# Optimization experiments

Hardware: AMD Instinct MI355X
Metric: run time of the kernel (lower is better)

## Reference

```python
import jax, jax.numpy as jnp
import numpy as np

B, H, W, C = 2, 64, 64, 256
NH, K = 8, 7  # num_heads, neighborhood kernel size


def setup_inputs() -> dict:
    key = jax.random.key(0)
    ks = jax.random.split(key, 8)
    xav = lambda k, shape: jax.random.normal(k, shape, jnp.float32) * np.sqrt(2.0 / (shape[0] + shape[1])).astype(np.float32)
    return {
        "x": jax.random.normal(ks[0], (B, H, W, C), jnp.float32),
        "norm1_g": jnp.ones((C,), jnp.float32),
        "norm1_b": jnp.zeros((C,), jnp.float32),
        "qkv_w": xav(ks[1], (3 * C, C)),
        "qkv_b": jnp.zeros((3 * C,), jnp.float32),
        "rpb": jax.random.normal(ks[2], (NH, 2 * K - 1, 2 * K - 1), jnp.float32) * 0.02,
        "proj_w": xav(ks[3], (C, C)),
        "proj_b": jnp.zeros((C,), jnp.float32),
        "norm2_g": jnp.ones((C,), jnp.float32),
        "norm2_b": jnp.zeros((C,), jnp.float32),
        "fc1_w": xav(ks[4], (4 * C, C)),
        "fc1_b": jnp.zeros((4 * C,), jnp.float32),
        "fc2_w": xav(ks[5], (C, 4 * C)),
        "fc2_b": jnp.zeros((C,), jnp.float32),
    }


def _layernorm(x, g, b, eps=1e-5):
    m = x.mean(-1, keepdims=True)
    v = jnp.mean((x - m) ** 2, axis=-1, keepdims=True)
    return (x - m) * jax.lax.rsqrt(v + eps) * g + b


def _nat2d(x, qkv_w, qkv_b, rpb, proj_w, proj_b):
    """Neighborhood attention 2D (NATTEN semantics: edge-clamped k x k windows,
    relative positional bias indexed by key_pos - query_pos + k - 1)."""
    b, h, w, c = x.shape
    nh = rpb.shape[0]
    k = (rpb.shape[1] + 1) // 2
    dh = c // nh
    qkv = (x @ qkv_w.T + qkv_b).reshape(b, h, w, 3, nh, dh)
    q = qkv[..., 0, :, :] * (dh ** -0.5)  # [b,h,w,nh,dh]
    kk = qkv[..., 1, :, :]
    vv = qkv[..., 2, :, :]
    # edge-clamped window starts per query row/col
    starts_h = jnp.clip(jnp.arange(h) - k // 2, 0, h - k)
    starts_w = jnp.clip(jnp.arange(w) - k // 2, 0, w - k)
    idx_h = starts_h[:, None] + jnp.arange(k)  # [h,k] key row indices
    idx_w = starts_w[:, None] + jnp.arange(k)  # [w,k] key col indices
    # gather neighborhoods -> [b,h,w,k,k,nh,dh]
    knb = kk[:, idx_h][:, :, :, idx_w].transpose(0, 1, 3, 2, 4, 5, 6)
    vnb = vv[:, idx_h][:, :, :, idx_w].transpose(0, 1, 3, 2, 4, 5, 6)
    attn = jnp.einsum('bijhd,bijklhd->bijhkl', q, knb)  # [b,h,w,nh,k,k]
    # relative positional bias: index = key - query + (k-1) in [0, 2k-2]
    rb_h = idx_h - jnp.arange(h)[:, None] + (k - 1)  # [h,k]
    rb_w = idx_w - jnp.arange(w)[:, None] + (k - 1)  # [w,k]
    bias = rpb[:, rb_h][:, :, :, rb_w]  # [nh,h,k,w,k]
    bias = bias.transpose(1, 3, 0, 2, 4)  # [h,w,nh,k,k]
    attn = jax.nn.softmax((attn + bias).reshape(b, h, w, nh, k * k), axis=-1)
    out = jnp.einsum('bijhn,bijnhd->bijhd', attn, vnb.reshape(b, h, w, k * k, nh, dh))
    return out.reshape(b, h, w, c) @ proj_w.T + proj_b


def reference(x, norm1_g, norm1_b, qkv_w, qkv_b, rpb, proj_w, proj_b,
              norm2_g, norm2_b, fc1_w, fc1_b, fc2_w, fc2_b):
    # norm -> neighborhood attention -> residual
    x = x + _nat2d(_layernorm(x, norm1_g, norm1_b), qkv_w, qkv_b, rpb, proj_w, proj_b)
    # norm -> MLP (gelu) -> residual
    hdn = _layernorm(x, norm2_g, norm2_b)
    hdn = jax.nn.gelu(hdn @ fc1_w.T + fc1_b, approximate=False)
    return x + (hdn @ fc2_w.T + fc2_b)
```

## Files before the change

kernel.cpp:

```cpp
#include <hip/hip_runtime.h>

typedef __attribute__((ext_vector_type(8))) short bf16x8;
typedef __attribute__((ext_vector_type(4))) float f32x4;
typedef unsigned short u16;

__device__ __forceinline__ float bf2f(u16 u) {
    return __builtin_bit_cast(float, ((unsigned int)u) << 16);
}
__device__ __forceinline__ u16 f2bf(float f) {
    unsigned int x = __builtin_bit_cast(unsigned int, f);
    x += 0x7FFFu + ((x >> 16) & 1u);
    return (u16)(x >> 16);
}

typedef const __attribute__((address_space(1))) void* gas_t;
typedef __attribute__((address_space(3))) void* las_t;
__device__ __forceinline__ void load_lds16(const u16* g, u16* l) {
    __builtin_amdgcn_global_load_lds((gas_t)g, (las_t)l, 16, 0, 0);
}

__global__ __launch_bounds__(256) void prep_kernel(
    const float* __restrict__ s0, const float* __restrict__ s1,
    const float* __restrict__ s2, const float* __restrict__ s3,
    u16* __restrict__ dst,
    const float* __restrict__ x, const float* __restrict__ g,
    const float* __restrict__ b, u16* __restrict__ y)
{
    if (blockIdx.x < 768) {
        const int i4 = (blockIdx.x * 256 + threadIdx.x) * 4;
        const float* src;
        int off;
        if      (i4 < 196608) { src = s0; off = i4; }
        else if (i4 < 262144) { src = s1; off = i4 - 196608; }
        else if (i4 < 524288) { src = s2; off = i4 - 262144; }
        else                  { src = s3; off = i4 - 524288; }
        float4 v = *(const float4*)(src + off);
        ushort4 o;
        o.x = f2bf(v.x); o.y = f2bf(v.y); o.z = f2bf(v.z); o.w = f2bf(v.w);
        *(ushort4*)(dst + i4) = o;
        return;
    }
    const int tok  = (blockIdx.x - 768) * 4 + (threadIdx.x >> 6);
    const int lane = threadIdx.x & 63;
    float4 v = *(const float4*)(x + (size_t)tok * 256 + lane * 4);
    float s  = v.x + v.y + v.z + v.w;
    float sq = v.x*v.x + v.y*v.y + v.z*v.z + v.w*v.w;
    #pragma unroll
    for (int off = 32; off; off >>= 1) {
        s  += __shfl_xor(s, off);
        sq += __shfl_xor(sq, off);
    }
    float mean = s * (1.0f / 256.0f);
    float var  = sq * (1.0f / 256.0f) - mean * mean;
    float rs   = rsqrtf(var + 1e-5f);
    float4 gv = *(const float4*)(g + lane * 4);
    float4 bv = *(const float4*)(b + lane * 4);
    ushort4 o;
    o.x = f2bf((v.x - mean) * rs * gv.x + bv.x);
    o.y = f2bf((v.y - mean) * rs * gv.y + bv.y);
    o.z = f2bf((v.z - mean) * rs * gv.z + bv.z);
    o.w = f2bf((v.w - mean) * rs * gv.w + bv.w);
    *(ushort4*)(y + (size_t)tok * 256 + lane * 4) = o;
}

template<int BM, int BN, int N, int K, int EPI>
__global__ __launch_bounds__(256) void gemm(
    const u16* __restrict__ A, const u16* __restrict__ W,
    const float* __restrict__ bias, const float* __restrict__ res,
    void* __restrict__ outv,
    const float* __restrict__ g2, const float* __restrict__ b2,
    u16* __restrict__ out2)
{
    constexpr int WMT = BM / 32;
    constexpr int WNT = BN / 32;
    constexpr int AR  = BM / 32;
    constexpr int BR  = BN / 32;

    __shared__ u16 As[BM * 64];
    __shared__ u16 Bs[BN * 64];
    __shared__ float red[2][2][16][2];
    const int tid  = threadIdx.x;
    const int lane = tid & 63;
    const int wave = tid >> 6;
    const int m0   = blockIdx.x * BM;
    const int n0   = blockIdx.y * BN;
    const int wm0  = (wave >> 1) * (BM / 2);
    const int wn0  = (wave & 1) * (BN / 2);

    f32x4 acc[WMT][WNT];
    #pragma unroll
    for (int mt = 0; mt < WMT; ++mt)
        #pragma unroll
        for (int nt = 0; nt < WNT; ++nt)
            acc[mt][nt] = (f32x4){0.f, 0.f, 0.f, 0.f};

    int soffA[AR];
    #pragma unroll
    for (int r = 0; r < AR; ++r) {
        const int s   = r * 256 + tid;
        const int row = s >> 3;
        const int c   = (s & 7) ^ (row & 7);
        soffA[r] = row * K + c * 8;
    }
    int soffB[BR];
    #pragma unroll
    for (int r = 0; r < BR; ++r) {
        const int s   = r * 256 + tid;
        const int row = s >> 3;
        const int c   = (s & 7) ^ (row & 7);
        soffB[r] = row * K + c * 8;
    }
    const int fr = lane & 15;
    const int fc = lane >> 4;

    for (int k0 = 0; k0 < K; k0 += 64) {
        __syncthreads();
        #pragma unroll
        for (int r = 0; r < AR; ++r)
            load_lds16(A + (size_t)m0 * K + k0 + soffA[r], As + (r * 256 + tid) * 8);
        #pragma unroll
        for (int r = 0; r < BR; ++r)
            load_lds16(W + (size_t)n0 * K + k0 + soffB[r], Bs + (r * 256 + tid) * 8);
        __syncthreads();
        #pragma unroll
        for (int ks = 0; ks < 2; ++ks) {
            bf16x8 af[WMT], bw[WNT];
            #pragma unroll
            for (int mt = 0; mt < WMT; ++mt) {
                const int rr   = wm0 + mt * 16 + fr;
                const int phys = (ks * 4 + fc) ^ (rr & 7);
                af[mt] = *(const bf16x8*)(As + rr * 64 + phys * 8);
            }
            #pragma unroll
            for (int nt = 0; nt < WNT; ++nt) {
                const int rr   = wn0 + nt * 16 + fr;
                const int phys = (ks * 4 + fc) ^ (rr & 7);
                bw[nt] = *(const bf16x8*)(Bs + rr * 64 + phys * 8);
            }
            #pragma unroll
            for (int mt = 0; mt < WMT; ++mt)
                #pragma unroll
                for (int nt = 0; nt < WNT; ++nt)
                    acc[mt][nt] = __builtin_amdgcn_mfma_f32_16x16x32_bf16(af[mt], bw[nt], acc[mt][nt], 0, 0, 0);
        }
    }

    const int col = lane & 15;
    const int rb  = (lane >> 4) * 4;

    if (EPI == 4) {
        float vv[WNT][4];
        float s[4]  = {0.f, 0.f, 0.f, 0.f};
        float sq[4] = {0.f, 0.f, 0.f, 0.f};
        #pragma unroll
        for (int nt = 0; nt < WNT; ++nt) {
            const int n  = n0 + wn0 + nt * 16 + col;
            const float bv = bias[n];
            #pragma unroll
            for (int r = 0; r < 4; ++r) {
                const int m = m0 + wm0 + rb + r;
                float v = acc[0][nt][r] + bv + res[(size_t)m * N + n];
                ((float*)outv)[(size_t)m * N + n] = v;
                vv[nt][r] = v;
                s[r]  += v;
                sq[r] += v * v;
            }
        }
        #pragma unroll
        for (int off = 1; off < 16; off <<= 1) {
            #pragma unroll
            for (int r = 0; r < 4; ++r) {
                s[r]  += __shfl_xor(s[r], off);
                sq[r] += __shfl_xor(sq[r], off);
            }
        }
        if ((lane & 15) == 0) {
            #pragma unroll
            for (int r = 0; r < 4; ++r) {
                red[wave >> 1][wave & 1][rb + r][0] = s[r];
                red[wave >> 1][wave & 1][rb + r][1] = sq[r];
            }
        }
        __syncthreads();
        float mean[4], rs[4];
        #pragma unroll
        for (int r = 0; r < 4; ++r) {
            float ts  = red[wave >> 1][0][rb + r][0] + red[wave >> 1][1][rb + r][0];
            float tsq = red[wave >> 1][0][rb + r][1] + red[wave >> 1][1][rb + r][1];
            mean[r] = ts * (1.0f / 256.0f);
            float var = tsq * (1.0f / 256.0f) - mean[r] * mean[r];
            rs[r] = rsqrtf(var + 1e-5f);
        }
        #pragma unroll
        for (int nt = 0; nt < WNT; ++nt) {
            const int n  = n0 + wn0 + nt * 16 + col;
            const float gv = g2[n];
            const float bv2 = b2[n];
            #pragma unroll
            for (int r = 0; r < 4; ++r) {
                const int m = m0 + wm0 + rb + r;
                out2[(size_t)m * 256 + n] = f2bf((vv[nt][r] - mean[r]) * rs[r] * gv + bv2);
            }
        }
        return;
    }

    #pragma unroll
    for (int nt = 0; nt < WNT; ++nt) {
        const int n  = n0 + wn0 + nt * 16 + col;
        const float bv = bias[n];
        #pragma unroll
        for (int mt = 0; mt < WMT; ++mt) {
            #pragma unroll
            for (int r = 0; r < 4; ++r) {
                const int m = m0 + wm0 + mt * 16 + rb + r;
                float v = acc[mt][nt][r] + bv;
                if (EPI == 1) {
                    if (n < 256) v *= 0.1767766952966369f;
                    ((u16*)outv)[(size_t)m * N + n] = f2bf(v);
                }
                if (EPI == 2) {
                    v += res[(size_t)m * N + n];
                    ((float*)outv)[(size_t)m * N + n] = v;
                }
                if (EPI == 3) {
                    v = 0.5f * v * (1.0f + erff(v * 0.7071067811865475f));
                    ((u16*)outv)[(size_t)m * N + n] = f2bf(v);
                }
            }
        }
    }
}

__global__ __launch_bounds__(64) void attn_mfma_kernel(
    const u16* __restrict__ qkv, const float* __restrict__ rpb,
    u16* __restrict__ out)
{
    __shared__ float rpbs[192];

    const int l = threadIdx.x;
    const int B = blockIdx.x;
    const int L = (B & 7) * 512 + (B >> 3);
    const int tile = L >> 3;
    const int h    = L & 7;
    const int bb   = tile >> 8;
    const int rem  = tile & 255;
    const int ti0  = (rem >> 4) << 2;
    const int tj0  = (rem & 15) << 2;
    const int oh   = min(max(ti0 - 3, 0), 54);
    const int ow   = min(max(tj0 - 3, 0), 54);
    const int tokbase = bb * 4096;

    #pragma unroll
    for (int r = 0; r < 3; ++r) {
        const int idx = r * 64 + l;
        rpbs[idx] = (idx < 169) ? rpb[h * 169 + idx] : -1e30f;
    }

    const int q = l & 15;
    const int g = l >> 4;

    const int tokq = tokbase + (ti0 + (q >> 2)) * 64 + (tj0 + (q & 3));
    const bf16x8 qf = *(const bf16x8*)(qkv + (size_t)tokq * 768 + h * 32 + g * 8);
    bf16x8 kf[7];
    #pragma unroll
    for (int t = 0; t < 7; ++t) {
        const int key = 16 * t + q;
        const int kkc = min(key, 99);
        const int tr  = (kkc * 205) >> 11, tc = kkc - tr * 10;
        const int tokg = tokbase + (oh + tr) * 64 + (ow + tc);
        kf[t] = *(const bf16x8*)(qkv + (size_t)tokg * 768 + 256 + h * 32 + g * 8);
    }

    const int i  = ti0 + (q >> 2), j = tj0 + (q & 3);
    const int sh = min(max(i - 3, 0), 57), sw = min(max(j - 3, 0), 57);
    const int khb = sh - oh, kwb = sw - ow;
    const int bh0 = oh - i + 6, bw0 = ow - j + 6;
    int bidx[7][4];
    int vtok[7][4];
    #pragma unroll
    for (int t = 0; t < 7; ++t)
        #pragma unroll
        for (int r = 0; r < 4; ++r) {
            const int kk  = 16 * t + 4 * g + r;
            const int kkc = min(kk, 99);
            const int hr  = (kkc * 205) >> 11;
            const int hc  = kkc - hr * 10;
            vtok[t][r] = tokbase + (oh + hr) * 64 + (ow + hc);
            const bool valid = (kk < 100)
                && ((unsigned)(hr - khb) < 7u) && ((unsigned)(hc - kwb) < 7u);
            bidx[t][r] = valid ? (bh0 + hr) * 13 + (bw0 + hc) : 169;
        }

    __syncthreads();

    f32x4 S[7];
    #pragma unroll
    for (int t = 0; t < 7; ++t)
        S[t] = __builtin_amdgcn_mfma_f32_16x16x32_bf16(kf[t], qf, (f32x4){0.f,0.f,0.f,0.f}, 0, 0, 0);

    float p[7][4];
    float mx = -1e30f;
    #pragma unroll
    for (int t = 0; t < 7; ++t)
        #pragma unroll
        for (int r = 0; r < 4; ++r) {
            const float v = S[t][r] + rpbs[bidx[t][r]];
            p[t][r] = v;
            mx = fmaxf(mx, v);
        }
    mx = fmaxf(mx, __shfl_xor(mx, 16));
    mx = fmaxf(mx, __shfl_xor(mx, 32));
    float sum = 0.f;
    #pragma unroll
    for (int t = 0; t < 7; ++t)
        #pragma unroll
        for (int r = 0; r < 4; ++r) {
            const float e = __expf(p[t][r] - mx);
            p[t][r] = e;
            sum += e;
        }
    sum += __shfl_xor(sum, 16);
    sum += __shfl_xor(sum, 32);
    const float inv = 1.f / sum;

    f32x4 O0 = {0.f,0.f,0.f,0.f}, O1 = {0.f,0.f,0.f,0.f};
    const u16* vbase = qkv + 512 + h * 32 + q;
    #pragma unroll
    for (int kt = 0; kt < 4; ++kt) {
        const int t0   = 2 * kt;
        const bool has1 = (2 * kt + 1) < 7;
        const int t1   = has1 ? 2 * kt + 1 : 2 * kt;
        bf16x8 ph, pl, vA, vB;
        #pragma unroll
        for (int jj = 0; jj < 4; ++jj) {
            const float a = p[t0][jj] * inv;
            const u16 ha = f2bf(a);
            ph[jj] = (short)ha;
            pl[jj] = (short)f2bf(a - bf2f(ha));
            const float b = has1 ? p[t1][jj] * inv : 0.f;
            const u16 hb = f2bf(b);
            ph[4 + jj] = (short)hb;
            pl[4 + jj] = (short)f2bf(b - bf2f(hb));
            vA[jj]     = (short)vbase[(size_t)vtok[t0][jj] * 768];
            vB[jj]     = (short)vbase[(size_t)vtok[t0][jj] * 768 + 16];
            vA[4 + jj] = (short)vbase[(size_t)vtok[t1][jj] * 768];
            vB[4 + jj] = (short)vbase[(size_t)vtok[t1][jj] * 768 + 16];
        }
        O0 = __builtin_amdgcn_mfma_f32_16x16x32_bf16(ph, vA, O0, 0, 0, 0);
        O0 = __builtin_amdgcn_mfma_f32_16x16x32_bf16(pl, vA, O0, 0, 0, 0);
        O1 = __builtin_amdgcn_mfma_f32_16x16x32_bf16(ph, vB, O1, 0, 0, 0);
        O1 = __builtin_amdgcn_mfma_f32_16x16x32_bf16(pl, vB, O1, 0, 0, 0);
    }

    #pragma unroll
    for (int r = 0; r < 4; ++r) {
        const int qq = g * 4 + r;
        const size_t base = (size_t)(tokbase + (ti0 + (qq >> 2)) * 64 + (tj0 + (qq & 3))) * 256
                          + h * 32 + q;
        out[base]      = f2bf(O0[r]);
        out[base + 16] = f2bf(O1[r]);
    }
}

extern "C" void kernel_launch(void* const* d_in, const int* in_sizes, int n_in,
                              void* d_out, int out_size, void* d_ws, size_t ws_size,
                              hipStream_t stream)
{
    const float* x      = (const float*)d_in[0];
    const float* n1g    = (const float*)d_in[1];
    const float* n1b    = (const float*)d_in[2];
    const float* qkv_w  = (const float*)d_in[3];
    const float* qkv_b  = (const float*)d_in[4];
    const float* rpb    = (const float*)d_in[5];
    const float* proj_w = (const float*)d_in[6];
    const float* proj_b = (const float*)d_in[7];
    const float* n2g    = (const float*)d_in[8];
    const float* n2b    = (const float*)d_in[9];
    const float* fc1_w  = (const float*)d_in[10];
    const float* fc1_b  = (const float*)d_in[11];
    const float* fc2_w  = (const float*)d_in[12];
    const float* fc2_b  = (const float*)d_in[13];
    float* out = (float*)d_out;

    char* wsb = (char*)d_ws;
    u16*   wbf   = (u16*)wsb;
    u16*   qkvW  = wbf;
    u16*   projW = wbf + 196608;
    u16*   fc1W  = wbf + 262144;
    u16*   fc2W  = wbf + 524288;
    u16*   ln1   = (u16*)(wsb + 1572864);
    u16*   attn  = ln1;
    u16*   qkvB  = (u16*)(wsb + 5767168);
    u16*   ln2   = qkvB;
    u16*   hbuf  = (u16*)(wsb + 9961472);
    float* x1    = (float*)(wsb + 26738688);

    dim3 blk(256);
    prep_kernel<<<2816, blk, 0, stream>>>(qkv_w, proj_w, fc1_w, fc2_w, wbf,
                                          x, n1g, n1b, ln1);
    gemm<128, 64, 768, 256, 1><<<dim3(64, 12), blk, 0, stream>>>(ln1, qkvW, qkv_b, nullptr, qkvB, nullptr, nullptr, nullptr);
    attn_mfma_kernel<<<4096, dim3(64), 0, stream>>>(qkvB, rpb, attn);
    gemm<32, 256, 256, 256, 4><<<dim3(256, 1), blk, 0, stream>>>(attn, projW, proj_b, x, x1, n2g, n2b, ln2);
    gemm<128, 64, 1024, 256, 3><<<dim3(64, 16), blk, 0, stream>>>(ln2, fc1W, fc1_b, nullptr, hbuf, nullptr, nullptr, nullptr);
    gemm<128, 64, 256, 1024, 2><<<dim3(64, 4), blk, 0, stream>>>(hbuf, fc2W, fc2_b, x1, out, nullptr, nullptr, nullptr);
}
```

Baseline: 151.4 us.

## Fuse neighborhood attention with output projection, residual and LayerNorm2

Merges the attention kernel with the projection GEMM epilogue. Each 512-thread block handles one 4x4 query tile, with 8 waves covering all heads. The attention output goes into swizzled LDS and is multiplied by projW, read directly from global memory. The block then adds bias and residual and computes LayerNorm2 in place. This removes a kernel launch and the global round trip of the attention output. In exchange there are fewer, larger blocks (512), and the projection weights are re-read from global memory by every block without LDS staging.

```diff
diff --git a/kernel.cpp b/kernel.cpp
--- a/kernel.cpp
+++ b/kernel.cpp
@@ -67,9 +67,7 @@
 __global__ __launch_bounds__(256) void gemm(
     const u16* __restrict__ A, const u16* __restrict__ W,
     const float* __restrict__ bias, const float* __restrict__ res,
-    void* __restrict__ outv,
-    const float* __restrict__ g2, const float* __restrict__ b2,
-    u16* __restrict__ out2)
+    void* __restrict__ outv)
 {
     constexpr int WMT = BM / 32;
     constexpr int WNT = BN / 32;
@@ -78,7 +76,6 @@
 
     __shared__ u16 As[BM * 64];
     __shared__ u16 Bs[BN * 64];
-    __shared__ float red[2][2][16][2];
     const int tid  = threadIdx.x;
     const int lane = tid & 63;
     const int wave = tid >> 6;
@@ -147,64 +144,6 @@
 
     const int col = lane & 15;
     const int rb  = (lane >> 4) * 4;
-
-    if (EPI == 4) {
-        float vv[WNT][4];
-        float s[4]  = {0.f, 0.f, 0.f, 0.f};
-        float sq[4] = {0.f, 0.f, 0.f, 0.f};
-        #pragma unroll
-        for (int nt = 0; nt < WNT; ++nt) {
-            const int n  = n0 + wn0 + nt * 16 + col;
-            const float bv = bias[n];
-            #pragma unroll
-            for (int r = 0; r < 4; ++r) {
-                const int m = m0 + wm0 + rb + r;
-                float v = acc[0][nt][r] + bv + res[(size_t)m * N + n];
-                ((float*)outv)[(size_t)m * N + n] = v;
-                vv[nt][r] = v;
-                s[r]  += v;
-                sq[r] += v * v;
-            }
-        }
-        #pragma unroll
-        for (int off = 1; off < 16; off <<= 1) {
-            #pragma unroll
-            for (int r = 0; r < 4; ++r) {
-                s[r]  += __shfl_xor(s[r], off);
-                sq[r] += __shfl_xor(sq[r], off);
-            }
-        }
-        if ((lane & 15) == 0) {
-            #pragma unroll
-            for (int r = 0; r < 4; ++r) {
-                red[wave >> 1][wave & 1][rb + r][0] = s[r];
-                red[wave >> 1][wave & 1][rb + r][1] = sq[r];
-            }
-        }
-        __syncthreads();
-        float mean[4], rs[4];
-        #pragma unroll
-        for (int r = 0; r < 4; ++r) {
-            float ts  = red[wave >> 1][0][rb + r][0] + red[wave >> 1][1][rb + r][0];
-            float tsq = red[wave >> 1][0][rb + r][1] + red[wave >> 1][1][rb + r][1];
-            mean[r] = ts * (1.0f / 256.0f);
-            float var = tsq * (1.0f / 256.0f) - mean[r] * mean[r];
-            rs[r] = rsqrtf(var + 1e-5f);
-        }
-        #pragma unroll
-        for (int nt = 0; nt < WNT; ++nt) {
-            const int n  = n0 + wn0 + nt * 16 + col;
-            const float gv = g2[n];
-            const float bv2 = b2[n];
-            #pragma unroll
-            for (int r = 0; r < 4; ++r) {
-                const int m = m0 + wm0 + rb + r;
-                out2[(size_t)m * 256 + n] = f2bf((vv[nt][r] - mean[r]) * rs[r] * gv + bv2);
-            }
-        }
-        return;
-    }
-
     #pragma unroll
     for (int nt = 0; nt < WNT; ++nt) {
         const int n  = n0 + wn0 + nt * 16 + col;
@@ -232,17 +171,22 @@
     }
 }
 
-__global__ __launch_bounds__(64) void attn_mfma_kernel(
+__global__ __launch_bounds__(512) void attn_proj_kernel(
     const u16* __restrict__ qkv, const float* __restrict__ rpb,
-    u16* __restrict__ out)
+    const u16* __restrict__ projW, const float* __restrict__ proj_b,
+    const float* __restrict__ xres, const float* __restrict__ g2,
+    const float* __restrict__ b2, float* __restrict__ x1,
+    u16* __restrict__ ln2)
 {
-    __shared__ float rpbs[192];
-
-    const int l = threadIdx.x;
-    const int B = blockIdx.x;
-    const int L = (B & 7) * 512 + (B >> 3);
-    const int tile = L >> 3;
-    const int h    = L & 7;
+    __shared__ u16   ao[16 * 256];
+    __shared__ float rpbs[8 * 177];
+    __shared__ float red[8][16][2];
+
+    const int tid = threadIdx.x;
+    const int l   = tid & 63;
+    const int w   = tid >> 6;
+    const int B   = blockIdx.x;
+    const int tile = (B & 7) * 64 + (B >> 3);
     const int bb   = tile >> 8;
     const int rem  = tile & 255;
     const int ti0  = (rem >> 4) << 2;
@@ -253,15 +197,19 @@
 
     #pragma unroll
     for (int r = 0; r < 3; ++r) {
-        const int idx = r * 64 + l;
-        rpbs[idx] = (idx < 169) ? rpb[h * 169 + idx] : -1e30f;
+        const int idx = r * 512 + tid;
+        if (idx < 1416) {
+            const int hh = idx / 177;
+            const int ii = idx - hh * 177;
+            rpbs[idx] = (ii < 169) ? rpb[hh * 169 + ii] : -1e30f;
+        }
     }
 
     const int q = l & 15;
     const int g = l >> 4;
 
     const int tokq = tokbase + (ti0 + (q >> 2)) * 64 + (tj0 + (q & 3));
-    const bf16x8 qf = *(const bf16x8*)(qkv + (size_t)tokq * 768 + h * 32 + g * 8);
+    const bf16x8 qf = *(const bf16x8*)(qkv + (size_t)tokq * 768 + w * 32 + g * 8);
     bf16x8 kf[7];
     #pragma unroll
     for (int t = 0; t < 7; ++t) {
@@ -269,7 +217,7 @@
         const int kkc = min(key, 99);
         const int tr  = (kkc * 205) >> 11, tc = kkc - tr * 10;
         const int tokg = tokbase + (oh + tr) * 64 + (ow + tc);
-        kf[t] = *(const bf16x8*)(qkv + (size_t)tokg * 768 + 256 + h * 32 + g * 8);
+        kf[t] = *(const bf16x8*)(qkv + (size_t)tokg * 768 + 256 + w * 32 + g * 8);
     }
 
     const int i  = ti0 + (q >> 2), j = tj0 + (q & 3);
@@ -299,13 +247,14 @@
     for (int t = 0; t < 7; ++t)
         S[t] = __builtin_amdgcn_mfma_f32_16x16x32_bf16(kf[t], qf, (f32x4){0.f,0.f,0.f,0.f}, 0, 0, 0);
 
+    const float* rpbh = rpbs + w * 177;
     float p[7][4];
     float mx = -1e30f;
     #pragma unroll
     for (int t = 0; t < 7; ++t)
         #pragma unroll
         for (int r = 0; r < 4; ++r) {
-            const float v = S[t][r] + rpbs[bidx[t][r]];
+            const float v = S[t][r] + rpbh[bidx[t][r]];
             p[t][r] = v;
             mx = fmaxf(mx, v);
         }
@@ -325,7 +274,7 @@
     const float inv = 1.f / sum;
 
     f32x4 O0 = {0.f,0.f,0.f,0.f}, O1 = {0.f,0.f,0.f,0.f};
-    const u16* vbase = qkv + 512 + h * 32 + q;
+    const u16* vbase = qkv + 512 + w * 32 + q;
     #pragma unroll
     for (int kt = 0; kt < 4; ++kt) {
         const int t0   = 2 * kt;
@@ -355,11 +304,92 @@
 
     #pragma unroll
     for (int r = 0; r < 4; ++r) {
-        const int qq = g * 4 + r;
-        const size_t base = (size_t)(tokbase + (ti0 + (qq >> 2)) * 64 + (tj0 + (qq & 3))) * 256
-                          + h * 32 + q;
-        out[base]      = f2bf(O0[r]);
-        out[base + 16] = f2bf(O1[r]);
+        const int row = g * 4 + r;
+        const int c0  = w * 4 + (q >> 3);
+        const int c1  = c0 + 2;
+        ao[row * 256 + ((c0 ^ (row & 7)) << 3) + (q & 7)] = f2bf(O0[r]);
+        ao[row * 256 + ((c1 ^ (row & 7)) << 3) + (q & 7)] = f2bf(O1[r]);
+    }
+    __syncthreads();
+
+    const int fr  = l & 15;
+    const int fc  = l >> 4;
+    const int n0w = w * 32;
+    f32x4 pacc[2];
+    pacc[0] = (f32x4){0.f,0.f,0.f,0.f};
+    pacc[1] = (f32x4){0.f,0.f,0.f,0.f};
+    #pragma unroll
+    for (int ks = 0; ks < 8; ++ks) {
+        const int physA = (ks * 4 + fc) ^ (fr & 7);
+        const bf16x8 af = *(const bf16x8*)(ao + fr * 256 + physA * 8);
+        #pragma unroll
+        for (int nt = 0; nt < 2; ++nt) {
+            const int n = n0w + nt * 16 + fr;
+            const bf16x8 bw = *(const bf16x8*)(projW + (size_t)n * 256 + ks * 32 + fc * 8);
+            pacc[nt] = __builtin_amdgcn_mfma_f32_16x16x32_bf16(af, bw, pacc[nt], 0, 0, 0);
+        }
+    }
+
+    const int col = l & 15;
+    const int rb  = (l >> 4) * 4;
+    float vv[2][4];
+    float s[4]  = {0.f, 0.f, 0.f, 0.f};
+    float sq[4] = {0.f, 0.f, 0.f, 0.f};
+    #pragma unroll
+    for (int nt = 0; nt < 2; ++nt) {
+        const int n = n0w + nt * 16 + col;
+        const float bv = proj_b[n];
+        #pragma unroll
+        for (int r = 0; r < 4; ++r) {
+            const int t = rb + r;
+            const size_t gi = (size_t)(tokbase + (ti0 + (t >> 2)) * 64 + (tj0 + (t & 3))) * 256 + n;
+            float v = pacc[nt][r] + bv + xres[gi];
+            x1[gi] = v;
+            vv[nt][r] = v;
+            s[r]  += v;
+            sq[r] += v * v;
+        }
+    }
+    #pragma unroll
+    for (int off = 1; off < 16; off <<= 1) {
+        #pragma unroll
+        for (int r = 0; r < 4; ++r) {
+            s[r]  += __shfl_xor(s[r], off);
+            sq[r] += __shfl_xor(sq[r], off);
+        }
+    }
+    if (col == 0) {
+        #pragma unroll
+        for (int r = 0; r < 4; ++r) {
+            red[w][rb + r][0] = s[r];
+            red[w][rb + r][1] = sq[r];
+        }
+    }
+    __syncthreads();
+    float mean[4], rsv[4];
+    #pragma unroll
+    for (int r = 0; r < 4; ++r) {
+        float ts = 0.f, tq = 0.f;
+        #pragma unroll
+        for (int ww = 0; ww < 8; ++ww) {
+            ts += red[ww][rb + r][0];
+            tq += red[ww][rb + r][1];
+        }
+        mean[r] = ts * (1.0f / 256.0f);
+        const float var = tq * (1.0f / 256.0f) - mean[r] * mean[r];
+        rsv[r]  = rsqrtf(var + 1e-5f);
+    }
+    #pragma unroll
+    for (int nt = 0; nt < 2; ++nt) {
+        const int n = n0w + nt * 16 + col;
+        const float gv  = g2[n];
+        const float bv2 = b2[n];
+        #pragma unroll
+        for (int r = 0; r < 4; ++r) {
+            const int t = rb + r;
+            const size_t gi = (size_t)(tokbase + (ti0 + (t >> 2)) * 64 + (tj0 + (t & 3))) * 256 + n;
+            ln2[gi] = f2bf((vv[nt][r] - mean[r]) * rsv[r] * gv + bv2);
+        }
     }
 }
 
@@ -390,18 +420,16 @@
     u16*   fc1W  = wbf + 262144;
     u16*   fc2W  = wbf + 524288;
     u16*   ln1   = (u16*)(wsb + 1572864);
-    u16*   attn  = ln1;
     u16*   qkvB  = (u16*)(wsb + 5767168);
-    u16*   ln2   = qkvB;
     u16*   hbuf  = (u16*)(wsb + 9961472);
     float* x1    = (float*)(wsb + 26738688);
+    u16*   ln2   = (u16*)(wsb + 35651584);
 
     dim3 blk(256);
     prep_kernel<<<2816, blk, 0, stream>>>(qkv_w, proj_w, fc1_w, fc2_w, wbf,
                                           x, n1g, n1b, ln1);
-    gemm<128, 64, 768, 256, 1><<<dim3(64, 12), blk, 0, stream>>>(ln1, qkvW, qkv_b, nullptr, qkvB, nullptr, nullptr, nullptr);
-    attn_mfma_kernel<<<4096, dim3(64), 0, stream>>>(qkvB, rpb, attn);
-    gemm<32, 256, 256, 256, 4><<<dim3(256, 1), blk, 0, stream>>>(attn, projW, proj_b, x, x1, n2g, n2b, ln2);
-    gemm<128, 64, 1024, 256, 3><<<dim3(64, 16), blk, 0, stream>>>(ln2, fc1W, fc1_b, nullptr, hbuf, nullptr, nullptr, nullptr);
-    gemm<128, 64, 256, 1024, 2><<<dim3(64, 4), blk, 0, stream>>>(hbuf, fc2W, fc2_b, x1, out, nullptr, nullptr, nullptr);
-}
+    gemm<128, 64, 768, 256, 1><<<dim3(64, 12), blk, 0, stream>>>(ln1, qkvW, qkv_b, nullptr, qkvB);
+    attn_proj_kernel<<<512, dim3(512), 0, stream>>>(qkvB, rpb, projW, proj_b, x, n2g, n2b, x1, ln2);
+    gemm<128, 64, 1024, 256, 3><<<dim3(64, 16), blk, 0, stream>>>(ln2, fc1W, fc1_b, nullptr, hbuf);
+    gemm<128, 64, 256, 1024, 2><<<dim3(64, 4), blk, 0, stream>>>(hbuf, fc2W, fc2_b, x1, out);
+}
```

After: 147.1 us. 2.8% less time.
